# Kernel tuning notes

Measured on AMD Instinct MI355X. Metric: run time of the kernel, lower is better.

Reference implementation:

```python
import jax, jax.numpy as jnp
import numpy as np

N, MAX_DEG, F_IN, F_OUT = 20000, 32, 128, 128
TRIM_RATIO = 0.45
N_NEIGH_THRESHOLD = 3


def setup_inputs() -> dict:
    key = jax.random.key(0)
    k_h, k_nbr, k_deg, k_w, k_b = jax.random.split(key, 5)
    h = jax.random.normal(k_h, (N, F_IN), dtype=jnp.float32)
    nbr = jax.random.randint(k_nbr, (N, MAX_DEG), 0, N, dtype=jnp.int32)
    # in-degree in [1, MAX_DEG] so every node has at least one neighbor
    deg = jax.random.randint(k_deg, (N,), 1, MAX_DEG + 1, dtype=jnp.int32)
    # GCN symmetric normalizer deg^-0.5, per node, shape [N, 1]
    norm = (deg.astype(jnp.float32) ** -0.5)[:, None]
    stdv = 1.0 / np.sqrt(F_OUT)
    weight = jax.random.uniform(k_w, (F_IN, F_OUT), jnp.float32, -stdv, stdv)
    bias = jax.random.uniform(k_b, (F_OUT,), jnp.float32, -stdv, stdv)
    return {"h": h, "norm": norm, "weight": weight, "bias": bias,
            "nbr": nbr, "deg": deg}


def reference(h, norm, weight, bias, nbr, deg):
    # h: [N,F] node features (dropout=0 so input_ft == dropped_h == h)
    # nbr: [N,D] padded src indices; deg: [N] valid neighbor counts; norm: [N,1]
    D = nbr.shape[1]
    slot = jnp.arange(D, dtype=deg.dtype)[None, :]            # [1,D]
    valid = slot < deg[:, None]                                # [N,D]

    h_nbr = h[nbr]                                             # [N,D,F] = mailbox input_ft
    msg = h_nbr * norm[nbr]                                    # [N,D,F] = mailbox m (src h * src norm)

    # padded slots -> +inf so they sort past all valid entries (ranks >= deg)
    big = jnp.asarray(jnp.finfo(h.dtype).max, h.dtype)
    ift = jnp.where(valid[..., None], h_nbr, big)
    sidx = jnp.argsort(ift, axis=1)                            # per-feature sort over neighbors
    gathered = jnp.take_along_axis(msg, sidx, axis=1)          # [N,D,F]

    n = deg                                                    # per-node n_neigh
    b_raw = n // 2 - (1 - n % 2)
    b_cap = jnp.floor(n.astype(jnp.float32) * TRIM_RATIO).astype(n.dtype)
    b = jnp.maximum(jnp.minimum(b_raw, b_cap), 1)              # trim count per node

    # keep sorted ranks in [b, n-b)
    sel = (slot >= b[:, None]) & (slot < (n - b)[:, None])     # [N,D]
    trimmed_sum = jnp.sum(gathered * sel[..., None].astype(h.dtype), axis=1)  # [N,F]

    self0 = h * norm                                           # dst h * dst norm (mailbox 'self'[:,0])
    alpha = (2 * b).astype(h.dtype)[:, None]
    accum_med = (trimmed_sum + self0 * alpha) * norm           # trim_compensate=True branch
    accum_small = (n.astype(h.dtype)[:, None] * self0) * norm  # n_neigh <= threshold branch
    accum = jnp.where((n <= N_NEIGH_THRESHOLD)[:, None], accum_small, accum_med)

    # NodeApplyModule_V2: linear + bias + relu
    out = jax.nn.relu(accum @ weight + bias)
    return out
```

## Files before the change

### kernel.cpp

```cpp
#include <hip/hip_runtime.h>
#include <hip/hip_fp16.h>
#include <cfloat>
#include <cmath>

#define N_NODES 20000
#define MAXD 32
#define F 128

#define MTILE 16
#define NBLK (N_NODES / MTILE)

typedef _Float16 half8 __attribute__((ext_vector_type(8)));
typedef float f32x4 __attribute__((ext_vector_type(4)));
typedef unsigned int u32x4 __attribute__((ext_vector_type(4)));
typedef unsigned short us8v __attribute__((ext_vector_type(8)));


template <int SZ, int NV>
__device__ __forceinline__ void oe_sort_n(float (&a)[SZ]) {
#pragma unroll
  for (int p = 1; p < SZ; p <<= 1) {
#pragma unroll
    for (int q = p; q >= 1; q >>= 1) {
#pragma unroll
      for (int j = q % p; j <= SZ - 1 - q; j += 2 * q) {
#pragma unroll
        for (int i = 0; i < q; ++i) {
          int x = i + j, y = i + j + q;
          if (y < NV && (x / (2 * p)) == (y / (2 * p))) {
            float mn = fminf(a[x], a[y]);
            float mx = fmaxf(a[x], a[y]);
            a[x] = mn;
            a[y] = mx;
          }
        }
      }
    }
  }
}

template <int N>
struct TrimB {
  static constexpr int b_raw = N / 2 - (1 - (N & 1));
  static constexpr int b_cap = (int)((float)N * 0.45f);
  static constexpr int b_min = b_raw < b_cap ? b_raw : b_cap;
  static constexpr int value = b_min > 1 ? b_min : 1;
};

template <int SZ, int N>
__device__ __forceinline__ float trimmed_sum_n(const float* __restrict__ h,
                                               const float* __restrict__ norm,
                                               const int* __restrict__ nbr_row,
                                               int f) {
  constexpr int B = TrimB<N>::value;
  constexpr int NB = N - B;

  float ko[SZ];
  float nrm[SZ];
  float k[SZ];
#pragma unroll
  for (int d = 0; d < N; ++d) {
    int src = nbr_row[d];
    nrm[d] = norm[src];
    ko[d] = h[src * F + f];
    k[d] = ko[d];
  }
#pragma unroll
  for (int d = N; d < SZ; ++d) k[d] = FLT_MAX;

  oe_sort_n<SZ, N>(k);

  const float lo  = k[B];
  const float hi  = k[NB - 1];
  const float lom = k[B - 1];
  const float him = k[NB];

  float sum = 0.f;
  if ((lom < lo) & (hi < him)) {
#pragma unroll
    for (int d = 0; d < N; ++d) {
      bool keep = (ko[d] >= lo) & (ko[d] <= hi);
      sum = fmaf(keep ? ko[d] : 0.f, nrm[d], sum);
    }
  } else {
    int c_lt_lo = 0, c_lt_hi = 0;
#pragma unroll
    for (int d = 0; d < N; ++d) {
      c_lt_lo += (ko[d] < lo) ? 1 : 0;
      c_lt_hi += (ko[d] < hi) ? 1 : 0;
    }
    int run_lo = 0, run_hi = 0;
#pragma unroll
    for (int d = 0; d < N; ++d) {
      const float kd = ko[d];
      const float m = kd * nrm[d];
      const bool eql = (kd == lo);
      const bool eqh = (kd == hi);
      const bool lh = (lo < hi);
      const bool btw = (kd > lo) & (kd < hi);
      const int r_lo = c_lt_lo + run_lo;
      const int r_hi = c_lt_hi + run_hi;
      const bool inc = btw
                     | (eql & (r_lo >= B) & (lh | (r_lo < NB)))
                     | (lh & eqh & (r_hi < NB));
      sum += inc ? m : 0.f;
      run_lo += eql ? 1 : 0;
      run_hi += eqh ? 1 : 0;
    }
  }
  return sum;
}

__device__ __forceinline__ unsigned int split_pack(float v) {
  _Float16 hi = (_Float16)v;
  _Float16 lo = (_Float16)(v - (float)hi);
  unsigned short hb = __builtin_bit_cast(unsigned short, hi);
  unsigned short lb = __builtin_bit_cast(unsigned short, lo);
  return (unsigned int)hb | ((unsigned int)lb << 16);
}

__global__ __launch_bounds__(256) void whl_prep(const float* __restrict__ W,
                                                _Float16* __restrict__ Whl) {
  const int e = blockIdx.x * 256 + threadIdx.x;
  const int n = e >> 7, k = e & 127;
  const float w = W[k * F + n];
  const _Float16 hi = (_Float16)w;
  Whl[e] = hi;
  Whl[16384 + e] = (_Float16)(w - (float)hi);
}

__global__ __launch_bounds__(256) void gcn_fused(
    const float* __restrict__ h, const float* __restrict__ norm,
    const int* __restrict__ nbr, const int* __restrict__ deg,
    const _Float16* __restrict__ Whl, const float* __restrict__ bias,
    float* __restrict__ out) {
  __shared__ unsigned int As[MTILE * F];
  const int tid = threadIdx.x;
  const int hw = __builtin_amdgcn_readfirstlane(tid) >> 7;
  const int f = tid & 127;

#pragma unroll 1
  for (int it = 0; it < 8; ++it) {
    const int nl = it * 2 + hw;
    const int i = blockIdx.x * MTILE + nl;
    const int n = deg[i];
    const float ni = norm[i];
    const float hif = h[i * F + f];

    float val;
    if (n <= 3) {
      val = (float)n * hif * ni * ni;
    } else {
      const int* nbr_row = nbr + i * MAXD;
      float ts;
      int b;
      switch (n) {
#define TS_CASE(NN, SS) \
        case NN: ts = trimmed_sum_n<SS, NN>(h, norm, nbr_row, f); b = TrimB<NN>::value; break;
        TS_CASE(4, 4)
        TS_CASE(5, 8) TS_CASE(6, 8) TS_CASE(7, 8) TS_CASE(8, 8)
        TS_CASE(9, 16) TS_CASE(10, 16) TS_CASE(11, 16) TS_CASE(12, 16)
        TS_CASE(13, 16) TS_CASE(14, 16) TS_CASE(15, 16) TS_CASE(16, 16)
        TS_CASE(17, 32) TS_CASE(18, 32) TS_CASE(19, 32) TS_CASE(20, 32)
        TS_CASE(21, 32) TS_CASE(22, 32) TS_CASE(23, 32) TS_CASE(24, 32)
        TS_CASE(25, 32) TS_CASE(26, 32) TS_CASE(27, 32) TS_CASE(28, 32)
        TS_CASE(29, 32) TS_CASE(30, 32) TS_CASE(31, 32)
        default: ts = trimmed_sum_n<32, 32>(h, norm, nbr_row, f); b = TrimB<32>::value; break;
#undef TS_CASE
      }
      val = (ts + hif * ni * (float)(2 * b)) * ni;
    }
    As[nl * F + (f ^ ((nl & 7) << 2))] = split_pack(val);
  }

  __syncthreads();

  const int lane = tid & 63;
  const int wv = tid >> 6;
  const int l16 = lane & 15;
  const int kg = lane >> 4;
  const int row0 = blockIdx.x * MTILE;
  const int colb = wv * 32;
  const int s = (l16 & 7) << 2;

  f32x4 acc[2];
  acc[0] = (f32x4){0.f, 0.f, 0.f, 0.f};
  acc[1] = (f32x4){0.f, 0.f, 0.f, 0.f};

#pragma unroll
  for (int kc = 0; kc < F; kc += 32) {
    const int k0 = kc + kg * 8;
    u32x4 p0 = *(const u32x4*)(As + l16 * F + ((k0 + 0) ^ s));
    u32x4 p1 = *(const u32x4*)(As + l16 * F + ((k0 + 4) ^ s));
    us8v s0 = __builtin_bit_cast(us8v, p0);
    us8v s1 = __builtin_bit_cast(us8v, p1);
    half8 ah = __builtin_bit_cast(half8,
        (us8v)__builtin_shufflevector(s0, s1, 0, 2, 4, 6, 8, 10, 12, 14));
    half8 al = __builtin_bit_cast(half8,
        (us8v)__builtin_shufflevector(s0, s1, 1, 3, 5, 7, 9, 11, 13, 15));
#pragma unroll
    for (int cf = 0; cf < 2; ++cf) {
      const int n = colb + cf * 16 + l16;
      half8 bh = *(const half8*)(Whl + n * F + k0);
      half8 bl = *(const half8*)(Whl + 16384 + n * F + k0);
      acc[cf] = __builtin_amdgcn_mfma_f32_16x16x32_f16(ah, bh, acc[cf], 0, 0, 0);
      acc[cf] = __builtin_amdgcn_mfma_f32_16x16x32_f16(ah, bl, acc[cf], 0, 0, 0);
      acc[cf] = __builtin_amdgcn_mfma_f32_16x16x32_f16(al, bh, acc[cf], 0, 0, 0);
    }
  }

#pragma unroll
  for (int cf = 0; cf < 2; ++cf) {
    const int col = colb + cf * 16 + l16;
    const float bv = bias[col];
#pragma unroll
    for (int r = 0; r < 4; ++r) {
      const int row = row0 + kg * 4 + r;
      out[(size_t)row * F + col] = fmaxf(acc[cf][r] + bv, 0.f);
    }
  }
}

extern "C" void kernel_launch(void* const* d_in, const int* in_sizes, int n_in,
                              void* d_out, int out_size, void* d_ws, size_t ws_size,
                              hipStream_t stream) {
  const float* h = (const float*)d_in[0];
  const float* norm = (const float*)d_in[1];
  const float* weight = (const float*)d_in[2];
  const float* bias = (const float*)d_in[3];
  const int* nbr = (const int*)d_in[4];
  const int* deg = (const int*)d_in[5];
  float* out = (float*)d_out;

  _Float16* Whl = (_Float16*)d_ws;

  whl_prep<<<64, 256, 0, stream>>>(weight, Whl);
  gcn_fused<<<NBLK, 256, 0, stream>>>(h, norm, nbr, deg, Whl, bias, out);
}
```

Measured before the change: 115.3 us.

## Software-pipeline neighbor gathers one node ahead of the trimmed-sum sort

Each thread now issues the neighbor feature and norm loads for the next node into a second register buffer while it sorts and trims the current node. The goal is to hide gather latency behind the sorting-network compute. The cost is 128 extra live floats per thread, which raises register pressure and may cut occupancy or cause spills. The unconditional register copy at the end of each iteration also adds moves.

```diff
diff --git a/kernel.cpp b/kernel.cpp
--- a/kernel.cpp
+++ b/kernel.cpp
@@ -48,23 +48,14 @@
 };
 
 template <int SZ, int N>
-__device__ __forceinline__ float trimmed_sum_n(const float* __restrict__ h,
-                                               const float* __restrict__ norm,
-                                               const int* __restrict__ nbr_row,
-                                               int f) {
+__device__ __forceinline__ float trimmed_sum_pre(const float (&ko)[32],
+                                                 const float (&nrm)[32]) {
   constexpr int B = TrimB<N>::value;
   constexpr int NB = N - B;
 
-  float ko[SZ];
-  float nrm[SZ];
   float k[SZ];
 #pragma unroll
-  for (int d = 0; d < N; ++d) {
-    int src = nbr_row[d];
-    nrm[d] = norm[src];
-    ko[d] = h[src * F + f];
-    k[d] = ko[d];
-  }
+  for (int d = 0; d < N; ++d) k[d] = ko[d];
 #pragma unroll
   for (int d = N; d < SZ; ++d) k[d] = FLT_MAX;
 
@@ -138,25 +129,59 @@
   const int tid = threadIdx.x;
   const int hw = __builtin_amdgcn_readfirstlane(tid) >> 7;
   const int f = tid & 127;
+  const int base = blockIdx.x * MTILE;
+
+  float koA[32], nrmA[32];
+  float koB[32], nrmB[32];
+
+  int n_cur;
+  {
+    const int i = base + hw;
+    n_cur = deg[i];
+    const int ne = (n_cur <= 3) ? 0 : n_cur;
+    const int* nr = nbr + i * MAXD;
+#pragma unroll
+    for (int d = 0; d < 32; ++d) {
+      if (d < ne) {
+        const int src = nr[d];
+        nrmA[d] = norm[src];
+        koA[d] = h[src * F + f];
+      }
+    }
+  }
 
 #pragma unroll 1
   for (int it = 0; it < 8; ++it) {
+    int n_next = 0;
+    if (it < 7) {
+      const int i_next = base + (it + 1) * 2 + hw;
+      n_next = deg[i_next];
+      const int ne = (n_next <= 3) ? 0 : n_next;
+      const int* nr = nbr + i_next * MAXD;
+#pragma unroll
+      for (int d = 0; d < 32; ++d) {
+        if (d < ne) {
+          const int src = nr[d];
+          nrmB[d] = norm[src];
+          koB[d] = h[src * F + f];
+        }
+      }
+    }
+
     const int nl = it * 2 + hw;
-    const int i = blockIdx.x * MTILE + nl;
-    const int n = deg[i];
+    const int i = base + nl;
     const float ni = norm[i];
     const float hif = h[i * F + f];
 
     float val;
-    if (n <= 3) {
-      val = (float)n * hif * ni * ni;
+    if (n_cur <= 3) {
+      val = (float)n_cur * hif * ni * ni;
     } else {
-      const int* nbr_row = nbr + i * MAXD;
       float ts;
       int b;
-      switch (n) {
+      switch (n_cur) {
 #define TS_CASE(NN, SS) \
-        case NN: ts = trimmed_sum_n<SS, NN>(h, norm, nbr_row, f); b = TrimB<NN>::value; break;
+        case NN: ts = trimmed_sum_pre<SS, NN>(koA, nrmA); b = TrimB<NN>::value; break;
         TS_CASE(4, 4)
         TS_CASE(5, 8) TS_CASE(6, 8) TS_CASE(7, 8) TS_CASE(8, 8)
         TS_CASE(9, 16) TS_CASE(10, 16) TS_CASE(11, 16) TS_CASE(12, 16)
@@ -165,12 +190,19 @@
         TS_CASE(21, 32) TS_CASE(22, 32) TS_CASE(23, 32) TS_CASE(24, 32)
         TS_CASE(25, 32) TS_CASE(26, 32) TS_CASE(27, 32) TS_CASE(28, 32)
         TS_CASE(29, 32) TS_CASE(30, 32) TS_CASE(31, 32)
-        default: ts = trimmed_sum_n<32, 32>(h, norm, nbr_row, f); b = TrimB<32>::value; break;
+        default: ts = trimmed_sum_pre<32, 32>(koA, nrmA); b = TrimB<32>::value; break;
 #undef TS_CASE
       }
       val = (ts + hif * ni * (float)(2 * b)) * ni;
     }
     As[nl * F + (f ^ ((nl & 7) << 2))] = split_pack(val);
+
+    n_cur = n_next;
+#pragma unroll
+    for (int d = 0; d < 32; ++d) {
+      koA[d] = koB[d];
+      nrmA[d] = nrmB[d];
+    }
   }
 
   __syncthreads();
@@ -179,7 +211,7 @@
   const int wv = tid >> 6;
   const int l16 = lane & 15;
   const int kg = lane >> 4;
-  const int row0 = blockIdx.x * MTILE;
+  const int row0 = base;
   const int colb = wv * 32;
   const int s = (l16 & 7) << 2;
 
```

New measurement: 213.1 us. +84.8%, slower.
